# Performance work log

Hardware: AMD Instinct MI355X
Metric: run time of the kernel (lower is better)

The kernel has to match this reference:

```python
import jax, jax.numpy as jnp
import numpy as np

# Module hyperparameters (from init_kwargs defaults)
SEQ_LEN = 250
MASK_RATIO = 0.6
NUM_SPANS = 3
SPAN_LEN = max(1, int(SEQ_LEN * MASK_RATIO / NUM_SPANS))  # 50
QRS_RADIUS = 30
CENTER = SEQ_LEN // 2  # 125
QRS_START = CENTER - QRS_RADIUS  # 95
QRS_END = CENTER + QRS_RADIUS    # 155
AVOID_PROB = 0.8
MAX_ATTEMPTS = 15


def setup_inputs() -> dict:
    key = jax.random.key(0)
    x = jax.random.normal(key, (16384, 12, SEQ_LEN), dtype=jnp.float32)
    return {"x": x}


def _span_starts(key, B):
    """Vectorized replacement for the host-side rejection-sampling loop.

    For each (batch, span): decide QRS avoidance, draw MAX_ATTEMPTS candidate
    starts at once, take the first valid one, fall back to a fresh draw if all
    attempts overlap the QRS zone (same semantics as the torch retry loop).
    """
    k1, k2, k3 = jax.random.split(key, 3)
    hi = max(1, SEQ_LEN - SPAN_LEN)  # exclusive upper bound = 200
    use_physio = jax.random.uniform(k1, (B, NUM_SPANS)) < AVOID_PROB
    cands = jax.random.randint(k2, (B, NUM_SPANS, MAX_ATTEMPTS), 0, hi)  # (B,S,A)
    ends = jnp.minimum(cands + SPAN_LEN, SEQ_LEN)
    no_overlap = (ends <= QRS_START) | (cands >= QRS_END)
    valid = no_overlap | (~use_physio[..., None])  # (B,S,A)
    first = jnp.argmax(valid, axis=-1)  # first valid attempt index
    chosen = jnp.take_along_axis(cands, first[..., None], axis=-1)[..., 0]
    fallback = jax.random.randint(k3, (B, NUM_SPANS), 0, hi)
    return jnp.where(valid.any(axis=-1), chosen, fallback)  # (B,S)


def reference(x):
    B, C, L = x.shape
    start = _span_starts(jax.random.key(42), B)          # (B, NUM_SPANS)
    end = jnp.minimum(start + SPAN_LEN, L)
    idx = jnp.arange(L)                                   # (L,)
    span_mask = (idx >= start[..., None]) & (idx < end[..., None])  # (B,S,L)
    masks = span_mask.any(axis=1)                         # (B, L) True where masked
    masked_x = x * (~masks)[:, None, :].astype(x.dtype)   # zero masked positions
    return masked_x, masks
```

## Files before the change

kernel.cpp:

```cpp
#include <hip/hip_runtime.h>
#include <stdint.h>

namespace {

constexpr int SEQ    = 250;
constexpr int SPAN   = 50;
constexpr int NSPANS = 3;
constexpr int NATT   = 15;
constexpr int QS     = 95;
constexpr int QE     = 155;
constexpr int NB     = 16384;
constexpr int NCH    = 12;
constexpr uint32_t HI = 200;

struct U2 { uint32_t a, b; };

__host__ __device__ constexpr U2 tf2x32(uint32_t k0, uint32_t k1,
                                        uint32_t x0, uint32_t x1) {
  uint32_t ks[3] = { k0, k1, k0 ^ k1 ^ 0x1BD11BDAu };
  uint32_t rot[2][4] = { {13u, 15u, 26u, 6u}, {17u, 29u, 16u, 24u} };
  x0 += ks[0];
  x1 += ks[1];
  for (int i = 0; i < 5; ++i) {
    for (int j = 0; j < 4; ++j) {
      uint32_t r = rot[i & 1][j];
      x0 += x1;
      x1 = (x1 << r) | (x1 >> (32u - r));
      x1 ^= x0;
    }
    x0 += ks[(i + 1) % 3];
    x1 += ks[(i + 2) % 3] + (uint32_t)(i + 1);
  }
  return U2{x0, x1};
}

constexpr U2 SK1 = tf2x32(0u, 42u, 0u, 0u);
constexpr U2 SK2 = tf2x32(0u, 42u, 0u, 1u);
constexpr U2 SK3 = tf2x32(0u, 42u, 0u, 2u);

constexpr U2 K2H = tf2x32(SK2.a, SK2.b, 0u, 0u);
constexpr U2 K2L = tf2x32(SK2.a, SK2.b, 0u, 1u);
constexpr U2 K3H = tf2x32(SK3.a, SK3.b, 0u, 0u);
constexpr U2 K3L = tf2x32(SK3.a, SK3.b, 0u, 1u);

__device__ __forceinline__ uint32_t rbit(U2 k, uint32_t idx) {
  U2 r = tf2x32(k.a, k.b, 0u, idx);
  return r.a ^ r.b;
}

__device__ __forceinline__ uint32_t draw200(uint32_t h, uint32_t l) {
  return ((h % HI) * 96u + (l % HI)) % HI;
}

__global__ void k_starts(int* __restrict__ starts) {
  constexpr uint32_t NU = (uint32_t)NB * NSPANS;
  int t = blockIdx.x * blockDim.x + threadIdx.x;
  if (t >= (int)NU) return;

  uint32_t ub = rbit(SK1, (uint32_t)t);
  float u = __uint_as_float((ub >> 9) | 0x3f800000u) - 1.0f;
  bool physio = (u < 0.8f);

  int chosen = -1;
  for (int a = 0; a < NATT; ++a) {
    uint32_t idx = (uint32_t)t * NATT + (uint32_t)a;
    uint32_t h = rbit(K2H, idx);
    uint32_t l = rbit(K2L, idx);
    int cand = (int)draw200(h, l);
    bool no_ov = (cand + SPAN <= QS) || (cand >= QE);
    if (no_ov || !physio) { chosen = cand; break; }
  }

  int st;
  if (chosen >= 0) {
    st = chosen;
  } else {
    uint32_t h = rbit(K3H, (uint32_t)t);
    uint32_t l = rbit(K3L, (uint32_t)t);
    st = (int)draw200(h, l);
  }
  starts[t] = st;
}

constexpr int NV4X = NB * NCH * SEQ / 4;
constexpr int NV4M = NB * SEQ / 4;
constexpr int NV4T = NV4X + NV4M;

__global__ void k_fused(const float4* __restrict__ x4, float4* __restrict__ o4,
                        float4* __restrict__ m4, const int* __restrict__ starts) {
  int tid = blockIdx.x * blockDim.x + threadIdx.x;
  if (tid < NV4X) {
    int f = tid << 2;
    int b = f / (NCH * SEQ);
    int r = f - b * (NCH * SEQ);
    int pos0 = r % SEQ;
    int s0 = starts[b * 3 + 0];
    int s1 = starts[b * 3 + 1];
    int s2 = starts[b * 3 + 2];
    bool mm[4];
    int nmask = 0;
#pragma unroll
    for (int j = 0; j < 4; ++j) {
      int p = pos0 + j;
      if (p >= SEQ) p -= SEQ;
      bool m = ((unsigned)(p - s0) < (unsigned)SPAN) ||
               ((unsigned)(p - s1) < (unsigned)SPAN) ||
               ((unsigned)(p - s2) < (unsigned)SPAN);
      mm[j] = m;
      nmask += (int)m;
    }
    if (nmask == 4) {
      o4[tid] = make_float4(0.0f, 0.0f, 0.0f, 0.0f);
    } else {
      float4 v = x4[tid];
      if (mm[0]) v.x = 0.0f;
      if (mm[1]) v.y = 0.0f;
      if (mm[2]) v.z = 0.0f;
      if (mm[3]) v.w = 0.0f;
      o4[tid] = v;
    }
  } else {
    int t = tid - NV4X;
    int f = t << 2;
    float vv[4];
#pragma unroll
    for (int j = 0; j < 4; ++j) {
      int i = f + j;
      int b = i / SEQ;
      int p = i - b * SEQ;
      bool m = ((unsigned)(p - starts[b * 3 + 0]) < (unsigned)SPAN) ||
               ((unsigned)(p - starts[b * 3 + 1]) < (unsigned)SPAN) ||
               ((unsigned)(p - starts[b * 3 + 2]) < (unsigned)SPAN);
      vv[j] = m ? 1.0f : 0.0f;
    }
    m4[t] = make_float4(vv[0], vv[1], vv[2], vv[3]);
  }
}

}

extern "C" void kernel_launch(void* const* d_in, const int* in_sizes, int n_in,
                              void* d_out, int out_size, void* d_ws, size_t ws_size,
                              hipStream_t stream) {
  const float* x = (const float*)d_in[0];
  float* out = (float*)d_out;
  float* mask_out = out + (size_t)NB * NCH * SEQ;
  int* starts = (int*)d_ws;

  k_starts<<<(NB * NSPANS + 255) / 256, 256, 0, stream>>>(starts);
  k_fused<<<NV4T / 256, 256, 0, stream>>>(
      (const float4*)x, (float4*)out, (float4*)mask_out, starts);
}
```

Measured before the change: 339.1 us.

## Fuse span-start RNG into per-batch masking kernel with shared-memory starts

Drops the separate start-computation kernel. A single kernel now runs one block per batch row: three threads compute the span starts with the Threefry RNG, the block syncs through shared memory, and then it masks the 12x250 slab and writes the mask row as float2. This removes a launch, the global round trip for starts and the per-element divisions, but every block now waits on a serial RNG loop of up to 15 attempts before streaming its data, and each 750-float4 slab leaves threads partly idle.

```diff
diff --git a/kernel.cpp b/kernel.cpp
--- a/kernel.cpp
+++ b/kernel.cpp
@@ -52,51 +52,39 @@
   return ((h % HI) * 96u + (l % HI)) % HI;
 }
 
-__global__ void k_starts(int* __restrict__ starts) {
-  constexpr uint32_t NU = (uint32_t)NB * NSPANS;
-  int t = blockIdx.x * blockDim.x + threadIdx.x;
-  if (t >= (int)NU) return;
+__device__ __forceinline__ int compute_start(uint32_t u) {
+  uint32_t ub = rbit(SK1, u);
+  float uu = __uint_as_float((ub >> 9) | 0x3f800000u) - 1.0f;
+  bool physio = (uu < 0.8f);
 
-  uint32_t ub = rbit(SK1, (uint32_t)t);
-  float u = __uint_as_float((ub >> 9) | 0x3f800000u) - 1.0f;
-  bool physio = (u < 0.8f);
-
-  int chosen = -1;
   for (int a = 0; a < NATT; ++a) {
-    uint32_t idx = (uint32_t)t * NATT + (uint32_t)a;
+    uint32_t idx = u * (uint32_t)NATT + (uint32_t)a;
     uint32_t h = rbit(K2H, idx);
     uint32_t l = rbit(K2L, idx);
     int cand = (int)draw200(h, l);
     bool no_ov = (cand + SPAN <= QS) || (cand >= QE);
-    if (no_ov || !physio) { chosen = cand; break; }
+    if (no_ov || !physio) return cand;
   }
-
-  int st;
-  if (chosen >= 0) {
-    st = chosen;
-  } else {
-    uint32_t h = rbit(K3H, (uint32_t)t);
-    uint32_t l = rbit(K3L, (uint32_t)t);
-    st = (int)draw200(h, l);
-  }
-  starts[t] = st;
+  uint32_t h = rbit(K3H, u);
+  uint32_t l = rbit(K3L, u);
+  return (int)draw200(h, l);
 }
 
-constexpr int NV4X = NB * NCH * SEQ / 4;
-constexpr int NV4M = NB * SEQ / 4;
-constexpr int NV4T = NV4X + NV4M;
+__global__ __launch_bounds__(256)
+void k_all(const float4* __restrict__ x4, float4* __restrict__ o4,
+           float2* __restrict__ m2) {
+  __shared__ int ss[NSPANS];
+  const int b = blockIdx.x;
+  const int t = threadIdx.x;
 
-__global__ void k_fused(const float4* __restrict__ x4, float4* __restrict__ o4,
-                        float4* __restrict__ m4, const int* __restrict__ starts) {
-  int tid = blockIdx.x * blockDim.x + threadIdx.x;
-  if (tid < NV4X) {
-    int f = tid << 2;
-    int b = f / (NCH * SEQ);
-    int r = f - b * (NCH * SEQ);
-    int pos0 = r % SEQ;
-    int s0 = starts[b * 3 + 0];
-    int s1 = starts[b * 3 + 1];
-    int s2 = starts[b * 3 + 2];
+  if (t < NSPANS) ss[t] = compute_start((uint32_t)(b * NSPANS + t));
+  __syncthreads();
+  const int s0 = ss[0], s1 = ss[1], s2 = ss[2];
+
+  const float4* xb = x4 + (size_t)b * (NCH * SEQ / 4);
+  float4*       ob = o4 + (size_t)b * (NCH * SEQ / 4);
+  for (int i = t; i < NCH * SEQ / 4; i += 256) {
+    int pos0 = (i << 2) % SEQ;
     bool mm[4];
     int nmask = 0;
 #pragma unroll
@@ -110,30 +98,28 @@
       nmask += (int)m;
     }
     if (nmask == 4) {
-      o4[tid] = make_float4(0.0f, 0.0f, 0.0f, 0.0f);
+      ob[i] = make_float4(0.0f, 0.0f, 0.0f, 0.0f);
     } else {
-      float4 v = x4[tid];
+      float4 v = xb[i];
       if (mm[0]) v.x = 0.0f;
       if (mm[1]) v.y = 0.0f;
       if (mm[2]) v.z = 0.0f;
       if (mm[3]) v.w = 0.0f;
-      o4[tid] = v;
+      ob[i] = v;
     }
-  } else {
-    int t = tid - NV4X;
-    int f = t << 2;
-    float vv[4];
-#pragma unroll
-    for (int j = 0; j < 4; ++j) {
-      int i = f + j;
-      int b = i / SEQ;
-      int p = i - b * SEQ;
-      bool m = ((unsigned)(p - starts[b * 3 + 0]) < (unsigned)SPAN) ||
-               ((unsigned)(p - starts[b * 3 + 1]) < (unsigned)SPAN) ||
-               ((unsigned)(p - starts[b * 3 + 2]) < (unsigned)SPAN);
-      vv[j] = m ? 1.0f : 0.0f;
-    }
-    m4[t] = make_float4(vv[0], vv[1], vv[2], vv[3]);
+  }
+
+  if (t < SEQ / 2) {
+    int p0 = t * 2;
+    bool ma = ((unsigned)(p0 - s0) < (unsigned)SPAN) ||
+              ((unsigned)(p0 - s1) < (unsigned)SPAN) ||
+              ((unsigned)(p0 - s2) < (unsigned)SPAN);
+    int p1 = p0 + 1;
+    bool mb = ((unsigned)(p1 - s0) < (unsigned)SPAN) ||
+              ((unsigned)(p1 - s1) < (unsigned)SPAN) ||
+              ((unsigned)(p1 - s2) < (unsigned)SPAN);
+    m2[(size_t)b * (SEQ / 2) + t] = make_float2(ma ? 1.0f : 0.0f,
+                                                mb ? 1.0f : 0.0f);
   }
 }
 
@@ -145,9 +131,7 @@
   const float* x = (const float*)d_in[0];
   float* out = (float*)d_out;
   float* mask_out = out + (size_t)NB * NCH * SEQ;
-  int* starts = (int*)d_ws;
 
-  k_starts<<<(NB * NSPANS + 255) / 256, 256, 0, stream>>>(starts);
-  k_fused<<<NV4T / 256, 256, 0, stream>>>(
-      (const float4*)x, (float4*)out, (float4*)mask_out, starts);
+  k_all<<<NB, 256, 0, stream>>>(
+      (const float4*)x, (float4*)out, (float2*)mask_out);
 }
```

After: 336.3 us. Within noise of the previous version (-0.8%).
